# Performance work log

Measured on AMD Instinct MI355X. Metric: run time of the kernel, lower is better.

The kernel has to match this reference:

```python
import jax, jax.numpy as jnp
import numpy as np

N_NODES = 10000
N_EDGES = 100000
DIM = 768
NEG_SLOPE = 0.2  # PyG GATConv default


def gat_conv(x, src, dst, W, att_src, att_dst, bias, num_nodes):
    """Single-head PyG-style GATConv. src/dst already include self-loops."""
    h = x @ W                                  # [N, D]
    a_s = h @ att_src                          # [N]
    a_d = h @ att_dst                          # [N]
    e = jax.nn.leaky_relu(a_s[src] + a_d[dst], NEG_SLOPE)  # [E']
    # segment softmax over edges sharing the same destination node
    m = jax.ops.segment_max(e, dst, num_segments=num_nodes)  # [N]
    e = jnp.exp(e - m[dst])
    denom = jax.ops.segment_sum(e, dst, num_segments=num_nodes)  # [N]
    alpha = e / denom[dst]                     # [E']
    msg = alpha[:, None] * h[src]              # [E', D]
    out = jax.ops.segment_sum(msg, dst, num_segments=num_nodes)  # [N, D]
    return out + bias


def setup_inputs() -> dict:
    key = jax.random.key(0)
    ks = jax.random.split(key, 12)
    s = 1.0 / np.sqrt(DIM)
    inp = {
        "x": jax.random.normal(ks[0], (N_NODES, DIM), dtype=jnp.float32),
        "edge_index": jax.random.randint(ks[1], (2, N_EDGES), 0, N_NODES, dtype=jnp.int64),
        "W1": jax.random.normal(ks[2], (DIM, DIM), dtype=jnp.float32) * s,
        "att_src1": jax.random.normal(ks[3], (DIM,), dtype=jnp.float32) * s,
        "att_dst1": jax.random.normal(ks[4], (DIM,), dtype=jnp.float32) * s,
        "b1": jnp.zeros((DIM,), dtype=jnp.float32),
        "W2": jax.random.normal(ks[5], (DIM, DIM), dtype=jnp.float32) * s,
        "att_src2": jax.random.normal(ks[6], (DIM,), dtype=jnp.float32) * s,
        "att_dst2": jax.random.normal(ks[7], (DIM,), dtype=jnp.float32) * s,
        "b2": jnp.zeros((DIM,), dtype=jnp.float32),
    }
    return inp


def reference(x, edge_index, W1, att_src1, att_dst1, b1, W2, att_src2, att_dst2, b2):
    n = x.shape[0]
    # PyG GATConv default add_self_loops=True
    loops = jnp.arange(n, dtype=edge_index.dtype)
    src = jnp.concatenate([edge_index[0], loops])
    dst = jnp.concatenate([edge_index[1], loops])
    h = gat_conv(x, src, dst, W1, att_src1, att_dst1, b1, n)
    h = jax.nn.relu(h)
    # dropout p=0.0 in eval -> identity
    out = gat_conv(h, src, dst, W2, att_src2, att_dst2, b2, n)
    return out
```

## Files before the change

### kernel.cpp

```cpp
#include <hip/hip_runtime.h>

#define DIM 768
#define NEG_SLOPE 0.2f

typedef unsigned short ushort_t;
typedef short short8 __attribute__((ext_vector_type(8)));
typedef float floatx4 __attribute__((ext_vector_type(4)));

__device__ __forceinline__ ushort_t f32_to_bf16(float f) {
  unsigned int b = __float_as_uint(f);
  b += 0x7FFFu + ((b >> 16) & 1u);
  return (ushort_t)(b >> 16);
}
__device__ __forceinline__ float bf16_to_f32(ushort_t u) {
  return __uint_as_float(((unsigned int)u) << 16);
}

__device__ __forceinline__ void gl2lds16(const ushort_t* g, ushort_t* l) {
  __builtin_amdgcn_global_load_lds(
      (const __attribute__((address_space(1))) void*)g,
      (__attribute__((address_space(3))) void*)l, 16, 0, 0);
}

__global__ void hist_kernel(const int* __restrict__ ei, int* __restrict__ deg,
                            int E, int Etot) {
  int e = blockIdx.x * 256 + threadIdx.x;
  if (e >= Etot) return;
  int d = (e < E) ? ei[E + e] : (e - E);
  atomicAdd(&deg[d], 1);
}

__global__ __launch_bounds__(256)
void scan_kernel(const int* __restrict__ deg, int* __restrict__ rowstart,
                 int* __restrict__ cursor, int n, int etot) {
  __shared__ int sdeg[10240];
  __shared__ int part[256];
  int tid = threadIdx.x;
  for (int i = tid; i < n; i += 256) sdeg[i] = deg[i];
  __syncthreads();
  int chunk = ((n + 255) / 256) | 1;
  int lo = min(tid * chunk, n);
  int hi = min(lo + chunk, n);
  int s = 0;
  for (int i = lo; i < hi; ++i) s += sdeg[i];
  part[tid] = s;
  __syncthreads();
  for (int off = 1; off < 256; off <<= 1) {
    int v = part[tid];
    int add = (tid >= off) ? part[tid - off] : 0;
    __syncthreads();
    part[tid] = v + add;
    __syncthreads();
  }
  int run = (tid == 0) ? 0 : part[tid - 1];
  for (int i = lo; i < hi; ++i) {
    int d = sdeg[i];
    sdeg[i] = run;
    run += d;
  }
  __syncthreads();
  for (int i = tid; i < n; i += 256) {
    int v = sdeg[i];
    rowstart[i] = v;
    cursor[i] = v;
  }
  if (tid == 0) rowstart[n] = etot;
}

__global__ void fill_kernel(const int* __restrict__ ei, int* __restrict__ cursor,
                            int* __restrict__ col, int E, int Etot) {
  int e = blockIdx.x * 256 + threadIdx.x;
  if (e >= Etot) return;
  int s, d;
  if (e < E) { s = ei[e]; d = ei[E + e]; }
  else       { s = e - E; d = e - E; }
  int pos = atomicAdd(&cursor[d], 1);
  col[pos] = s;
}

__global__ __launch_bounds__(256)
void prep_kernel(const float* __restrict__ x, ushort_t* __restrict__ xb, int n4,
                 const float* __restrict__ W1, ushort_t* __restrict__ wT1,
                 const float* __restrict__ W2, ushort_t* __restrict__ wT2) {
  int i = blockIdx.x * 256 + threadIdx.x;
  if (i < n4) {
    float4 v = ((const float4*)x)[i];
    ushort4 o;
    o.x = f32_to_bf16(v.x); o.y = f32_to_bf16(v.y);
    o.z = f32_to_bf16(v.z); o.w = f32_to_bf16(v.w);
    ((ushort4*)xb)[i] = o;
  }
  if (i < DIM * DIM) {
    int nrow = i / DIM;
    int k = i - nrow * DIM;
    wT1[i] = f32_to_bf16(W1[k * DIM + nrow]);
    wT2[i] = f32_to_bf16(W2[k * DIM + nrow]);
  }
}

__global__ __launch_bounds__(256)
void gemm_kernel(const ushort_t* __restrict__ A, const ushort_t* __restrict__ Bt,
                 const float* __restrict__ att_s, const float* __restrict__ att_d,
                 float* __restrict__ a_s, float* __restrict__ a_d,
                 ushort_t* __restrict__ Hb, int M) {
  const int K = DIM;
  __shared__ __align__(16) ushort_t As[128 * 32];
  __shared__ __align__(16) ushort_t Bs[128 * 32];
  int tid = threadIdx.x;
  int m0 = blockIdx.x * 128, n0 = blockIdx.y * 128;
  int wave = tid >> 6, lane = tid & 63;
  int wm = (wave & 1) * 64, wn = (wave >> 1) * 64;
  int quad = lane >> 4, l16 = lane & 15;

  floatx4 acc[4][4];
  const floatx4 fzero = {0.f, 0.f, 0.f, 0.f};
#pragma unroll
  for (int i = 0; i < 4; ++i)
#pragma unroll
    for (int j = 0; j < 4; ++j) acc[i][j] = fzero;

  int r0 = tid >> 2, c0 = tid & 3;
  int r1 = r0 + 64;
  int kc0 = ((c0 ^ ((r0 + (r0 >> 2)) & 3))) * 8;
  int kc1 = ((c0 ^ ((r1 + (r1 >> 2)) & 3))) * 8;

  const ushort_t* gA0 = A + (size_t)min(m0 + r0, M - 1) * K + kc0;
  const ushort_t* gA1 = A + (size_t)min(m0 + r1, M - 1) * K + kc1;
  const ushort_t* gB0 = Bt + (size_t)(n0 + r0) * K + kc0;
  const ushort_t* gB1 = Bt + (size_t)(n0 + r1) * K + kc1;
  ushort_t* lA0 = As + wave * 512;
  ushort_t* lA1 = As + 2048 + wave * 512;
  ushort_t* lB0 = Bs + wave * 512;
  ushort_t* lB1 = Bs + 2048 + wave * 512;

  for (int k0 = 0; k0 < K; k0 += 32) {
    gl2lds16(gA0 + k0, lA0);
    gl2lds16(gA1 + k0, lA1);
    gl2lds16(gB0 + k0, lB0);
    gl2lds16(gB1 + k0, lB1);
    __syncthreads();

    short8 af[4], bfr[4];
#pragma unroll
    for (int i = 0; i < 4; ++i) {
      int ra = wm + i * 16 + l16;
      int qa = quad ^ ((ra + (ra >> 2)) & 3);
      af[i] = *(const short8*)(As + ra * 32 + qa * 8);
      int rb = wn + i * 16 + l16;
      int qb = quad ^ ((rb + (rb >> 2)) & 3);
      bfr[i] = *(const short8*)(Bs + rb * 32 + qb * 8);
    }
#pragma unroll
    for (int i = 0; i < 4; ++i)
#pragma unroll
      for (int j = 0; j < 4; ++j)
        acc[i][j] = __builtin_amdgcn_mfma_f32_16x16x32_bf16(af[i], bfr[j], acc[i][j], 0, 0, 0);
    __syncthreads();
  }

  float avs[4], avd[4];
#pragma unroll
  for (int j = 0; j < 4; ++j) {
    int c = n0 + wn + j * 16 + l16;
    avs[j] = att_s[c];
    avd[j] = att_d[c];
  }

#pragma unroll
  for (int i = 0; i < 4; ++i) {
#pragma unroll
    for (int r = 0; r < 4; ++r) {
      int row = m0 + wm + i * 16 + quad * 4 + r;
      bool valid = row < M;
      float pvs = 0.f, pvd = 0.f;
#pragma unroll
      for (int j = 0; j < 4; ++j) {
        float v = acc[i][j][r];
        if (valid) Hb[(size_t)row * DIM + n0 + wn + j * 16 + l16] = f32_to_bf16(v);
        pvs = fmaf(v, avs[j], pvs);
        pvd = fmaf(v, avd[j], pvd);
      }
#pragma unroll
      for (int off = 1; off < 16; off <<= 1) {
        pvs += __shfl_xor(pvs, off, 64);
        pvd += __shfl_xor(pvd, off, 64);
      }
      if (valid && l16 == 0) {
        atomicAdd(a_s + row, pvs);
        atomicAdd(a_d + row, pvd);
      }
    }
  }
}

__global__ __launch_bounds__(256)
void aggregate_kernel(const ushort_t* __restrict__ h, const float* __restrict__ a_s,
                      const float* __restrict__ a_d, const int* __restrict__ rowstart,
                      const int* __restrict__ col, const float* __restrict__ bias,
                      float* __restrict__ out_f32, ushort_t* __restrict__ out_bf16,
                      int relu_mode, int N) {
  int wave = threadIdx.x >> 6, lane = threadIdx.x & 63;
  int node = blockIdx.x * 4 + wave;
  if (node >= N) return;
  int start = rowstart[node], end = rowstart[node + 1];
  float ad = a_d[node];

  float vmax = -3.4e38f;
  for (int e = start + lane; e < end; e += 64) {
    float v = a_s[col[e]] + ad;
    v = (v > 0.f) ? v : NEG_SLOPE * v;
    vmax = fmaxf(vmax, v);
  }
#pragma unroll
  for (int off = 32; off > 0; off >>= 1) vmax = fmaxf(vmax, __shfl_xor(vmax, off, 64));

  float ssum = 0.f;
  for (int e = start + lane; e < end; e += 64) {
    float v = a_s[col[e]] + ad;
    v = (v > 0.f) ? v : NEG_SLOPE * v;
    ssum += __expf(v - vmax);
  }
#pragma unroll
  for (int off = 32; off > 0; off >>= 1) ssum += __shfl_xor(ssum, off, 64);
  float inv = 1.f / ssum;

  float acc[3][4];
#pragma unroll
  for (int q = 0; q < 3; ++q)
#pragma unroll
    for (int k = 0; k < 4; ++k) acc[q][k] = 0.f;

  for (int base = start; base < end; base += 64) {
    int e = base + lane;
    float al = 0.f;
    int sc = 0;
    if (e < end) {
      sc = col[e];
      float v = a_s[sc] + ad;
      v = (v > 0.f) ? v : NEG_SLOPE * v;
      al = __expf(v - vmax) * inv;
    }
    int cnt = min(64, end - base);
    for (int j = 0; j < cnt; ++j) {
      float w = __shfl(al, j, 64);
      int s = __shfl(sc, j, 64);
      const ushort_t* hr = h + (size_t)s * DIM;
#pragma unroll
      for (int q = 0; q < 3; ++q) {
        ushort4 u = *(const ushort4*)(hr + 4 * (lane + 64 * q));
        acc[q][0] = fmaf(w, bf16_to_f32(u.x), acc[q][0]);
        acc[q][1] = fmaf(w, bf16_to_f32(u.y), acc[q][1]);
        acc[q][2] = fmaf(w, bf16_to_f32(u.z), acc[q][2]);
        acc[q][3] = fmaf(w, bf16_to_f32(u.w), acc[q][3]);
      }
    }
  }

  size_t ob = (size_t)node * DIM;
#pragma unroll
  for (int q = 0; q < 3; ++q) {
    int c = 4 * (lane + 64 * q);
    float4 bv = *(const float4*)(bias + c);
    float o0 = acc[q][0] + bv.x;
    float o1 = acc[q][1] + bv.y;
    float o2 = acc[q][2] + bv.z;
    float o3 = acc[q][3] + bv.w;
    if (relu_mode) {
      ushort4 st;
      st.x = f32_to_bf16(fmaxf(o0, 0.f));
      st.y = f32_to_bf16(fmaxf(o1, 0.f));
      st.z = f32_to_bf16(fmaxf(o2, 0.f));
      st.w = f32_to_bf16(fmaxf(o3, 0.f));
      *(ushort4*)(out_bf16 + ob + c) = st;
    } else {
      float4 st = make_float4(o0, o1, o2, o3);
      *(float4*)(out_f32 + ob + c) = st;
    }
  }
}

extern "C" void kernel_launch(void* const* d_in, const int* in_sizes, int n_in,
                              void* d_out, int out_size, void* d_ws, size_t ws_size,
                              hipStream_t stream) {
  const float* x   = (const float*)d_in[0];
  const int*   ei  = (const int*)d_in[1];
  const float* W1  = (const float*)d_in[2];
  const float* as1 = (const float*)d_in[3];
  const float* ad1 = (const float*)d_in[4];
  const float* b1  = (const float*)d_in[5];
  const float* W2  = (const float*)d_in[6];
  const float* as2 = (const float*)d_in[7];
  const float* ad2 = (const float*)d_in[8];
  const float* b2  = (const float*)d_in[9];

  const int N = in_sizes[0] / DIM;
  const int E = in_sizes[1] / 2;
  const int Etot = E + N;

  char* p = (char*)d_ws;
  auto alloc = [&](size_t bytes) {
    char* q = p;
    p += (bytes + 255) & ~(size_t)255;
    return q;
  };
  ushort_t* Hb     = (ushort_t*)alloc((size_t)N * DIM * 2);
  ushort_t* xb     = (ushort_t*)alloc((size_t)N * DIM * 2);
  ushort_t* wT1    = (ushort_t*)alloc((size_t)DIM * DIM * 2);
  ushort_t* wT2    = (ushort_t*)alloc((size_t)DIM * DIM * 2);
  int*      zbase  = (int*)alloc((size_t)5 * N * 4);
  int*      deg    = zbase;
  float*    a_s1   = (float*)(zbase + N);
  float*    a_d1   = (float*)(zbase + 2 * N);
  float*    a_s2   = (float*)(zbase + 3 * N);
  float*    a_d2   = (float*)(zbase + 4 * N);
  int*      rowst  = (int*)alloc((size_t)(N + 1) * 4);
  int*      cursor = (int*)alloc((size_t)N * 4);
  int*      col    = (int*)alloc((size_t)Etot * 4);

  hipMemsetAsync(zbase, 0, (size_t)5 * N * 4, stream);
  prep_kernel<<<(N * DIM / 4 + 255) / 256, 256, 0, stream>>>(x, xb, N * DIM / 4,
                                                             W1, wT1, W2, wT2);
  hist_kernel<<<(Etot + 255) / 256, 256, 0, stream>>>(ei, deg, E, Etot);
  scan_kernel<<<1, 256, 0, stream>>>(deg, rowst, cursor, N, Etot);
  fill_kernel<<<(Etot + 255) / 256, 256, 0, stream>>>(ei, cursor, col, E, Etot);

  dim3 ggrid((N + 127) / 128, DIM / 128);

  gemm_kernel<<<ggrid, 256, 0, stream>>>(xb, wT1, as1, ad1, a_s1, a_d1, Hb, N);
  aggregate_kernel<<<(N + 3) / 4, 256, 0, stream>>>(Hb, a_s1, a_d1, rowst, col, b1,
                                                    nullptr, xb, 1, N);
  gemm_kernel<<<ggrid, 256, 0, stream>>>(xb, wT2, as2, ad2, a_s2, a_d2, Hb, N);
  aggregate_kernel<<<(N + 3) / 4, 256, 0, stream>>>(Hb, a_s2, a_d2, rowst, col, b2,
                                                    (float*)d_out, nullptr, 0, N);
}
```

Before: 244.0 us.

## Deepen GEMM K-tile to 64, widen aggregate loads, fold memset into prep

The GEMM now stages 64-wide K slices per iteration with an XOR swizzle over 8 chunks, which halves the number of barrier pairs per tile and doubles LDS use. The aggregate kernel switches from three 8-byte loads per row to one 16-byte and one 8-byte load, and stores packed bf16 pairs. The separate memset is removed, and zeroing the degree and attention buffers is folded into the prep kernel to save a launch. The higher LDS footprint may lower GEMM occupancy.

```diff
diff --git a/kernel.cpp b/kernel.cpp
--- a/kernel.cpp
+++ b/kernel.cpp
@@ -15,11 +15,42 @@
 __device__ __forceinline__ float bf16_to_f32(ushort_t u) {
   return __uint_as_float(((unsigned int)u) << 16);
 }
+__device__ __forceinline__ float bf16lo(unsigned int u) {
+  return __uint_as_float(u << 16);
+}
+__device__ __forceinline__ float bf16hi(unsigned int u) {
+  return __uint_as_float(u & 0xFFFF0000u);
+}
+__device__ __forceinline__ unsigned int pack_bf16x2(float lo, float hi) {
+  return ((unsigned int)f32_to_bf16(lo)) | (((unsigned int)f32_to_bf16(hi)) << 16);
+}
 
 __device__ __forceinline__ void gl2lds16(const ushort_t* g, ushort_t* l) {
   __builtin_amdgcn_global_load_lds(
       (const __attribute__((address_space(1))) void*)g,
       (__attribute__((address_space(3))) void*)l, 16, 0, 0);
+}
+
+__global__ __launch_bounds__(256)
+void prep_kernel(const float* __restrict__ x, ushort_t* __restrict__ xb, int n4,
+                 const float* __restrict__ W1, ushort_t* __restrict__ wT1,
+                 const float* __restrict__ W2, ushort_t* __restrict__ wT2,
+                 int* __restrict__ zbase, int nz) {
+  int i = blockIdx.x * 256 + threadIdx.x;
+  if (i < n4) {
+    float4 v = ((const float4*)x)[i];
+    ushort4 o;
+    o.x = f32_to_bf16(v.x); o.y = f32_to_bf16(v.y);
+    o.z = f32_to_bf16(v.z); o.w = f32_to_bf16(v.w);
+    ((ushort4*)xb)[i] = o;
+  }
+  if (i < DIM * DIM) {
+    int nrow = i / DIM;
+    int k = i - nrow * DIM;
+    wT1[i] = f32_to_bf16(W1[k * DIM + nrow]);
+    wT2[i] = f32_to_bf16(W2[k * DIM + nrow]);
+  }
+  if (i < nz) zbase[i] = 0;
 }
 
 __global__ void hist_kernel(const int* __restrict__ ei, int* __restrict__ deg,
@@ -79,33 +110,13 @@
 }
 
 __global__ __launch_bounds__(256)
-void prep_kernel(const float* __restrict__ x, ushort_t* __restrict__ xb, int n4,
-                 const float* __restrict__ W1, ushort_t* __restrict__ wT1,
-                 const float* __restrict__ W2, ushort_t* __restrict__ wT2) {
-  int i = blockIdx.x * 256 + threadIdx.x;
-  if (i < n4) {
-    float4 v = ((const float4*)x)[i];
-    ushort4 o;
-    o.x = f32_to_bf16(v.x); o.y = f32_to_bf16(v.y);
-    o.z = f32_to_bf16(v.z); o.w = f32_to_bf16(v.w);
-    ((ushort4*)xb)[i] = o;
-  }
-  if (i < DIM * DIM) {
-    int nrow = i / DIM;
-    int k = i - nrow * DIM;
-    wT1[i] = f32_to_bf16(W1[k * DIM + nrow]);
-    wT2[i] = f32_to_bf16(W2[k * DIM + nrow]);
-  }
-}
-
-__global__ __launch_bounds__(256)
 void gemm_kernel(const ushort_t* __restrict__ A, const ushort_t* __restrict__ Bt,
                  const float* __restrict__ att_s, const float* __restrict__ att_d,
                  float* __restrict__ a_s, float* __restrict__ a_d,
                  ushort_t* __restrict__ Hb, int M) {
   const int K = DIM;
-  __shared__ __align__(16) ushort_t As[128 * 32];
-  __shared__ __align__(16) ushort_t Bs[128 * 32];
+  __shared__ __align__(16) ushort_t As[128 * 64];
+  __shared__ __align__(16) ushort_t Bs[128 * 64];
   int tid = threadIdx.x;
   int m0 = blockIdx.x * 128, n0 = blockIdx.y * 128;
   int wave = tid >> 6, lane = tid & 63;
@@ -119,42 +130,45 @@
 #pragma unroll
     for (int j = 0; j < 4; ++j) acc[i][j] = fzero;
 
-  int r0 = tid >> 2, c0 = tid & 3;
-  int r1 = r0 + 64;
-  int kc0 = ((c0 ^ ((r0 + (r0 >> 2)) & 3))) * 8;
-  int kc1 = ((c0 ^ ((r1 + (r1 >> 2)) & 3))) * 8;
-
-  const ushort_t* gA0 = A + (size_t)min(m0 + r0, M - 1) * K + kc0;
-  const ushort_t* gA1 = A + (size_t)min(m0 + r1, M - 1) * K + kc1;
-  const ushort_t* gB0 = Bt + (size_t)(n0 + r0) * K + kc0;
-  const ushort_t* gB1 = Bt + (size_t)(n0 + r1) * K + kc1;
-  ushort_t* lA0 = As + wave * 512;
-  ushort_t* lA1 = As + 2048 + wave * 512;
-  ushort_t* lB0 = Bs + wave * 512;
-  ushort_t* lB1 = Bs + 2048 + wave * 512;
-
-  for (int k0 = 0; k0 < K; k0 += 32) {
-    gl2lds16(gA0 + k0, lA0);
-    gl2lds16(gA1 + k0, lA1);
-    gl2lds16(gB0 + k0, lB0);
-    gl2lds16(gB1 + k0, lB1);
+  int lr = lane >> 3, lc = lane & 7;
+  const ushort_t* gA[4];
+  const ushort_t* gB[4];
+  ushort_t* lA[4];
+  ushort_t* lB[4];
+#pragma unroll
+  for (int t = 0; t < 4; ++t) {
+    int r = t * 32 + wave * 8 + lr;
+    int g = lc ^ (r & 7);
+    gA[t] = A + (size_t)min(m0 + r, M - 1) * K + g * 8;
+    gB[t] = Bt + (size_t)(n0 + r) * K + g * 8;
+    lA[t] = As + (t * 32 + wave * 8) * 64;
+    lB[t] = Bs + (t * 32 + wave * 8) * 64;
+  }
+
+  for (int k0 = 0; k0 < K; k0 += 64) {
+#pragma unroll
+    for (int t = 0; t < 4; ++t) {
+      gl2lds16(gA[t] + k0, lA[t]);
+      gl2lds16(gB[t] + k0, lB[t]);
+    }
     __syncthreads();
 
-    short8 af[4], bfr[4];
-#pragma unroll
-    for (int i = 0; i < 4; ++i) {
-      int ra = wm + i * 16 + l16;
-      int qa = quad ^ ((ra + (ra >> 2)) & 3);
-      af[i] = *(const short8*)(As + ra * 32 + qa * 8);
-      int rb = wn + i * 16 + l16;
-      int qb = quad ^ ((rb + (rb >> 2)) & 3);
-      bfr[i] = *(const short8*)(Bs + rb * 32 + qb * 8);
-    }
-#pragma unroll
-    for (int i = 0; i < 4; ++i)
-#pragma unroll
-      for (int j = 0; j < 4; ++j)
-        acc[i][j] = __builtin_amdgcn_mfma_f32_16x16x32_bf16(af[i], bfr[j], acc[i][j], 0, 0, 0);
+#pragma unroll
+    for (int h = 0; h < 2; ++h) {
+      short8 af[4], bfr[4];
+#pragma unroll
+      for (int i = 0; i < 4; ++i) {
+        int ra = wm + i * 16 + l16;
+        af[i] = *(const short8*)(As + ra * 64 + ((((h << 2) | quad)) ^ (ra & 7)) * 8);
+        int rb = wn + i * 16 + l16;
+        bfr[i] = *(const short8*)(Bs + rb * 64 + ((((h << 2) | quad)) ^ (rb & 7)) * 8);
+      }
+#pragma unroll
+      for (int i = 0; i < 4; ++i)
+#pragma unroll
+        for (int j = 0; j < 4; ++j)
+          acc[i][j] = __builtin_amdgcn_mfma_f32_16x16x32_bf16(af[i], bfr[j], acc[i][j], 0, 0, 0);
+    }
     __syncthreads();
   }
 
@@ -224,11 +238,12 @@
   for (int off = 32; off > 0; off >>= 1) ssum += __shfl_xor(ssum, off, 64);
   float inv = 1.f / ssum;
 
-  float acc[3][4];
-#pragma unroll
-  for (int q = 0; q < 3; ++q)
-#pragma unroll
-    for (int k = 0; k < 4; ++k) acc[q][k] = 0.f;
+  float acc8[8];
+  float acc4[4];
+#pragma unroll
+  for (int k = 0; k < 8; ++k) acc8[k] = 0.f;
+#pragma unroll
+  for (int k = 0; k < 4; ++k) acc4[k] = 0.f;
 
   for (int base = start; base < end; base += 64) {
     int e = base + lane;
@@ -245,37 +260,52 @@
       float w = __shfl(al, j, 64);
       int s = __shfl(sc, j, 64);
       const ushort_t* hr = h + (size_t)s * DIM;
-#pragma unroll
-      for (int q = 0; q < 3; ++q) {
-        ushort4 u = *(const ushort4*)(hr + 4 * (lane + 64 * q));
-        acc[q][0] = fmaf(w, bf16_to_f32(u.x), acc[q][0]);
-        acc[q][1] = fmaf(w, bf16_to_f32(u.y), acc[q][1]);
-        acc[q][2] = fmaf(w, bf16_to_f32(u.z), acc[q][2]);
-        acc[q][3] = fmaf(w, bf16_to_f32(u.w), acc[q][3]);
-      }
+      uint4 u = *(const uint4*)(hr + lane * 8);
+      ushort4 t = *(const ushort4*)(hr + 512 + lane * 4);
+      acc8[0] = fmaf(w, bf16lo(u.x), acc8[0]);
+      acc8[1] = fmaf(w, bf16hi(u.x), acc8[1]);
+      acc8[2] = fmaf(w, bf16lo(u.y), acc8[2]);
+      acc8[3] = fmaf(w, bf16hi(u.y), acc8[3]);
+      acc8[4] = fmaf(w, bf16lo(u.z), acc8[4]);
+      acc8[5] = fmaf(w, bf16hi(u.z), acc8[5]);
+      acc8[6] = fmaf(w, bf16lo(u.w), acc8[6]);
+      acc8[7] = fmaf(w, bf16hi(u.w), acc8[7]);
+      acc4[0] = fmaf(w, bf16_to_f32(t.x), acc4[0]);
+      acc4[1] = fmaf(w, bf16_to_f32(t.y), acc4[1]);
+      acc4[2] = fmaf(w, bf16_to_f32(t.z), acc4[2]);
+      acc4[3] = fmaf(w, bf16_to_f32(t.w), acc4[3]);
     }
   }
 
   size_t ob = (size_t)node * DIM;
-#pragma unroll
-  for (int q = 0; q < 3; ++q) {
-    int c = 4 * (lane + 64 * q);
-    float4 bv = *(const float4*)(bias + c);
-    float o0 = acc[q][0] + bv.x;
-    float o1 = acc[q][1] + bv.y;
-    float o2 = acc[q][2] + bv.z;
-    float o3 = acc[q][3] + bv.w;
-    if (relu_mode) {
-      ushort4 st;
-      st.x = f32_to_bf16(fmaxf(o0, 0.f));
-      st.y = f32_to_bf16(fmaxf(o1, 0.f));
-      st.z = f32_to_bf16(fmaxf(o2, 0.f));
-      st.w = f32_to_bf16(fmaxf(o3, 0.f));
-      *(ushort4*)(out_bf16 + ob + c) = st;
-    } else {
-      float4 st = make_float4(o0, o1, o2, o3);
-      *(float4*)(out_f32 + ob + c) = st;
-    }
+  int c8 = lane * 8, c4 = 512 + lane * 4;
+  float4 b0 = *(const float4*)(bias + c8);
+  float4 b1 = *(const float4*)(bias + c8 + 4);
+  float4 b2 = *(const float4*)(bias + c4);
+  float o[12];
+  o[0] = acc8[0] + b0.x; o[1] = acc8[1] + b0.y;
+  o[2] = acc8[2] + b0.z; o[3] = acc8[3] + b0.w;
+  o[4] = acc8[4] + b1.x; o[5] = acc8[5] + b1.y;
+  o[6] = acc8[6] + b1.z; o[7] = acc8[7] + b1.w;
+  o[8] = acc4[0] + b2.x; o[9] = acc4[1] + b2.y;
+  o[10] = acc4[2] + b2.z; o[11] = acc4[3] + b2.w;
+  if (relu_mode) {
+#pragma unroll
+    for (int k = 0; k < 12; ++k) o[k] = fmaxf(o[k], 0.f);
+    uint4 s0;
+    s0.x = pack_bf16x2(o[0], o[1]);
+    s0.y = pack_bf16x2(o[2], o[3]);
+    s0.z = pack_bf16x2(o[4], o[5]);
+    s0.w = pack_bf16x2(o[6], o[7]);
+    *(uint4*)(out_bf16 + ob + c8) = s0;
+    uint2 s1;
+    s1.x = pack_bf16x2(o[8], o[9]);
+    s1.y = pack_bf16x2(o[10], o[11]);
+    *(uint2*)(out_bf16 + ob + c4) = s1;
+  } else {
+    *(float4*)(out_f32 + ob + c8) = make_float4(o[0], o[1], o[2], o[3]);
+    *(float4*)(out_f32 + ob + c8 + 4) = make_float4(o[4], o[5], o[6], o[7]);
+    *(float4*)(out_f32 + ob + c4) = make_float4(o[8], o[9], o[10], o[11]);
   }
 }
 
@@ -317,9 +347,8 @@
   int*      cursor = (int*)alloc((size_t)N * 4);
   int*      col    = (int*)alloc((size_t)Etot * 4);
 
-  hipMemsetAsync(zbase, 0, (size_t)5 * N * 4, stream);
-  prep_kernel<<<(N * DIM / 4 + 255) / 256, 256, 0, stream>>>(x, xb, N * DIM / 4,
-                                                             W1, wT1, W2, wT2);
+  prep_kernel<<<(N * DIM / 4 + 255) / 256, 256, 0, stream>>>(
+      x, xb, N * DIM / 4, W1, wT1, W2, wT2, zbase, 5 * N);
   hist_kernel<<<(Etot + 255) / 256, 256, 0, stream>>>(ei, deg, E, Etot);
   scan_kernel<<<1, 256, 0, stream>>>(deg, rowst, cursor, N, Etot);
   fill_kernel<<<(Etot + 255) / 256, 256, 0, stream>>>(ei, cursor, col, E, Etot);
```

Result: faster. 233.4 us (-4.4%).
